# Kernel optimization log

Hardware: AMD Instinct MI355X
Metric: run time of the kernel (lower is better)

The kernel has to match this reference:

```python
import jax, jax.numpy as jnp
import numpy as np

N, E, G, F = 100000, 3200000, 256, 15
NEG_SLOPE = 0.2


def _lin(k, fi, fo):
    s = 1.0 / np.sqrt(fi)
    return jax.random.uniform(k, (fi, fo), jnp.float32, -s, s)


def _vec(k, n, fi):
    s = 1.0 / np.sqrt(fi)
    return jax.random.uniform(k, (n,), jnp.float32, -s, s)


def setup_inputs() -> dict:
    key = jax.random.key(0)
    ks = jax.random.split(key, 40)
    inp = {}
    inp["x"] = jax.random.normal(ks[0], (N, F), jnp.float32)
    inp["edge_index"] = jax.random.randint(ks[1], (2, E), 0, N, dtype=jnp.int32)
    inp["batch"] = jnp.sort(jax.random.randint(ks[2], (N,), 0, G, dtype=jnp.int32))
    inp["xA"] = jax.random.normal(ks[3], (G, 300), jnp.float32)
    i = 4
    for l in (1, 2, 3):
        inp[f"cW{l}"] = _lin(ks[i], F, F); i += 1
        inp[f"cas{l}"] = _vec(ks[i], F, F); i += 1
        inp[f"cad{l}"] = _vec(ks[i], F, F); i += 1
        inp[f"cb{l}"] = jnp.zeros((F,), jnp.float32)
        inp[f"fW{l}"] = _lin(ks[i], F, F); i += 1
        inp[f"fb{l}"] = _vec(ks[i], F, F); i += 1
    inp["m1W"] = _lin(ks[i], 90, 90); i += 1
    inp["m1b"] = _vec(ks[i], 90, 90); i += 1
    inp["aW1"] = _lin(ks[i], 300, 300); i += 1
    inp["ab1"] = _vec(ks[i], 300, 300); i += 1
    inp["aW2"] = _lin(ks[i], 300, 300); i += 1
    inp["ab2"] = _vec(ks[i], 300, 300); i += 1
    inp["aW3"] = _lin(ks[i], 300, 300); i += 1
    inp["ab3"] = _vec(ks[i], 300, 300); i += 1
    inp["aW4"] = _lin(ks[i], 300, 45); i += 1
    inp["ab4"] = _vec(ks[i], 45, 300); i += 1
    inp["m2W"] = _lin(ks[i], 90, 1); i += 1
    inp["m2b"] = _vec(ks[i], 1, 90); i += 1
    return inp


def _gat(x, src, dst, W, a_s, a_d, b):
    """PyG GATConv (heads=1, add_self_loops handled by caller via src/dst)."""
    h = x @ W                                        # [N, F]
    e = jax.nn.leaky_relu((h @ a_s)[src] + (h @ a_d)[dst], NEG_SLOPE)  # [E+N]
    mx = jax.ops.segment_max(e, dst, num_segments=N)
    ex = jnp.exp(e - mx[dst])
    den = jax.ops.segment_sum(ex, dst, num_segments=N)
    alpha = ex / (den[dst] + 1e-16)                   # segment softmax over dst
    out = jax.ops.segment_sum(h[src] * alpha[:, None], dst, num_segments=N)
    return out + b


def reference(x, edge_index, batch, xA,
              cW1, cas1, cad1, cb1, fW1, fb1,
              cW2, cas2, cad2, cb2, fW2, fb2,
              cW3, cas3, cad3, cb3, fW3, fb3,
              m1W, m1b, aW1, ab1, aW2, ab2, aW3, ab3, aW4, ab4,
              m2W, m2b):
    loop = jnp.arange(N, dtype=edge_index.dtype)      # self loops
    src = jnp.concatenate([edge_index[0], loop])
    dst = jnp.concatenate([edge_index[1], loop])

    h = _gat(x, src, dst, cW1, cas1, cad1, cb1)
    h = jax.nn.relu(h @ fW1 + fb1)
    h = _gat(h, src, dst, cW2, cas2, cad2, cb2)
    h = jax.nn.relu(h @ fW2 + fb2)
    h = _gat(h, src, dst, cW3, cas3, cad3, cb3)
    h = h @ fW3 + fb3

    s = jax.ops.segment_sum(h, batch, num_segments=G)
    mx = jax.ops.segment_max(h, batch, num_segments=G)
    cnt = jax.ops.segment_sum(jnp.ones((N, 1), h.dtype), batch, num_segments=G)
    mean = s / jnp.maximum(cnt, 1.0)
    pooled = jnp.concatenate([s, mx, mean], axis=1)   # [G, 45]

    a = jax.nn.relu(xA @ aW1 + ab1)
    a = jax.nn.relu(a @ aW2 + ab2)
    a = jax.nn.sigmoid(a @ aW3 + ab3)
    xann = a @ aW4 + ab4                              # [G, 45]

    z = jnp.concatenate([pooled, xann], axis=1)       # [G, 90]
    z = jax.nn.relu(z @ m1W + m1b)
    z = z @ m2W + m2b
    return jax.nn.sigmoid(z)
```

## Files before the change

kernel.cpp:

```cpp
#include <hip/hip_runtime.h>
#include <hip/hip_bf16.h>
#include <math.h>

#define FDIM 15
#define FPAD 16
#define NEG_SLOPE 0.2f
#define BSH 8
#define BWID 256
#define HB_GRID 256
#define HB_BLK 1024

typedef _Float16 half_t;

__device__ __forceinline__ float leaky(float e) {
  return fmaxf(NEG_SLOPE * e, e);
}

__global__ void k_zero(int* __restrict__ p, int n) {
  int i = blockIdx.x * blockDim.x + threadIdx.x;
  if (i < n) p[i] = 0;
}

__global__ void k_bhist(const int* __restrict__ dstI, int* __restrict__ bcnt,
                        int* __restrict__ bhistG,
                        int n_tot, int n_real, int NB) {
  __shared__ int hist[512];
  int tid = threadIdx.x;
  for (int i = tid; i < NB; i += blockDim.x) hist[i] = 0;
  __syncthreads();
  int stride = gridDim.x * blockDim.x;
  for (int i = blockIdx.x * blockDim.x + tid; i < n_tot; i += stride) {
    int d = (i < n_real) ? dstI[i] : (i - n_real);
    atomicAdd(&hist[d >> BSH], 1);
  }
  __syncthreads();
  for (int i = tid; i < NB; i += blockDim.x) {
    int h = hist[i];
    bhistG[blockIdx.x * 512 + i] = h;
    if (h) atomicAdd(&bcnt[i], h);
  }
}

__global__ void k_bscan(const int* __restrict__ bcnt, int* __restrict__ boff,
                        int* __restrict__ bcur, int* __restrict__ rowptr,
                        int NB, int N, int total) {
  __shared__ int s[512];
  int tid = threadIdx.x;
  int v = (tid < NB) ? bcnt[tid] : 0;
  s[tid] = v;
  __syncthreads();
  for (int off = 1; off < 512; off <<= 1) {
    int add = (tid >= off) ? s[tid - off] : 0;
    __syncthreads();
    s[tid] += add;
    __syncthreads();
  }
  if (tid < NB) { int e = s[tid] - v; boff[tid] = e; bcur[tid] = e; }
  if (tid == NB - 1) boff[NB] = s[tid];
  if (tid == 0) rowptr[N] = total;
}

__global__ void k_bpart(const int* __restrict__ srcI, const int* __restrict__ dstI,
                        int* __restrict__ bcur, int* __restrict__ bbuf,
                        const int* __restrict__ bhistG,
                        int n_tot, int n_real, int NB) {
  __shared__ int hist[512];
  __shared__ int base[512];
  int tid = threadIdx.x;
  for (int i = tid; i < NB; i += blockDim.x) {
    int h = bhistG[blockIdx.x * 512 + i];
    base[i] = h ? atomicAdd(&bcur[i], h) : 0;
    hist[i] = 0;
  }
  __syncthreads();
  int stride = gridDim.x * blockDim.x;
  int g0 = blockIdx.x * blockDim.x + tid;
  for (int i = g0; i < n_tot; i += stride) {
    int s, d;
    if (i < n_real) { s = srcI[i]; d = dstI[i]; }
    else { s = d = i - n_real; }
    int b = d >> BSH;
    int p = base[b] + atomicAdd(&hist[b], 1);
    bbuf[p] = (s << BSH) | (d & (BWID - 1));
  }
}

__global__ void k_bbuild(const int* __restrict__ boff, const int* __restrict__ bbuf,
                         int* __restrict__ rowptr, int* __restrict__ csr, int N) {
  __shared__ int hist[BWID];
  __shared__ int sc[BWID];
  int b = blockIdx.x;
  int tid = threadIdx.x;
  int base_dst = b << BSH;
  int nd = min(BWID, N - base_dst);
  int s0 = boff[b], s1 = boff[b + 1];
  if (tid < BWID) hist[tid] = 0;
  __syncthreads();
  for (int j = s0 + tid; j < s1; j += 512)
    atomicAdd(&hist[bbuf[j] & (BWID - 1)], 1);
  __syncthreads();
  int v = 0;
  if (tid < BWID) { v = hist[tid]; sc[tid] = v; }
  __syncthreads();
  for (int off = 1; off < BWID; off <<= 1) {
    int add = 0;
    if (tid < BWID && tid >= off) add = sc[tid - off];
    __syncthreads();
    if (tid < BWID) sc[tid] += add;
    __syncthreads();
  }
  if (tid < nd) rowptr[base_dst + tid] = s0 + sc[tid] - v;
  __syncthreads();
  if (tid < BWID) hist[tid] = sc[tid] - v;
  __syncthreads();
  for (int j = s0 + tid; j < s1; j += 512) {
    int e = bbuf[j];
    int dl = e & (BWID - 1);
    int p = s0 + atomicAdd(&hist[dl], 1);
    csr[p] = (e >> BSH) << 5;
  }
}

__global__ void k_transform(const float* __restrict__ in, int ld_in,
                            const float* __restrict__ W,
                            const float* __restrict__ a_s,
                            const float* __restrict__ a_d,
                            half_t* __restrict__ hp,
                            float* __restrict__ ad_,
                            int n_nodes) {
  __shared__ float Ws[FDIM * FDIM];
  __shared__ float asv[FDIM], adv[FDIM];
  int tid = threadIdx.x;
  if (tid < FDIM * FDIM) Ws[tid] = W[tid];
  if (tid < FDIM) { asv[tid] = a_s[tid]; adv[tid] = a_d[tid]; }
  __syncthreads();
  int n = blockIdx.x * blockDim.x + tid;
  if (n >= n_nodes) return;
  float xin[FDIM];
#pragma unroll
  for (int j = 0; j < FDIM; ++j) xin[j] = in[n * ld_in + j];
  float sa = 0.f, da = 0.f;
  half_t hrow[FPAD];
#pragma unroll
  for (int o = 0; o < FDIM; ++o) {
    float acc = 0.f;
#pragma unroll
    for (int k = 0; k < FDIM; ++k) acc += xin[k] * Ws[k * FDIM + o];
    hrow[o] = (half_t)acc;
    sa += acc * asv[o];
    da += acc * adv[o];
  }
  hrow[FDIM] = (half_t)sa;
  ad_[n] = da;
  float4 w0, w1;
  __builtin_memcpy(&w0, &hrow[0], 16);
  __builtin_memcpy(&w1, &hrow[8], 16);
  float4* dst = (float4*)(hp + (size_t)n * FPAD);
  dst[0] = w0;
  dst[1] = w1;
}

__device__ __forceinline__ void mlp_rider(int g, int tid, int nthreads,
                                          const float* __restrict__ mIn,
                                          const float* __restrict__ mW,
                                          const float* __restrict__ mB,
                                          float* __restrict__ mOut,
                                          int Nout, int mAct,
                                          float* mins) {
  for (int k = tid; k < 300; k += nthreads) mins[k] = mIn[(size_t)g * 300 + k];
  __syncthreads();
  int j1 = tid;
  int j2 = tid + nthreads;
  bool p1 = (j1 < Nout), p2 = (j2 < Nout);
  if (!p1) return;
  float a0 = 0.f, a1 = 0.f, a2 = 0.f, a3 = 0.f;
  float a4 = 0.f, a5 = 0.f, a6 = 0.f, a7 = 0.f;
  float b0 = 0.f, b1 = 0.f, b2 = 0.f, b3 = 0.f;
  float b4 = 0.f, b5 = 0.f, b6 = 0.f, b7 = 0.f;
  int k = 0;
  for (; k + 7 < 300; k += 8) {
    float i0 = mins[k],     i1 = mins[k + 1], i2 = mins[k + 2], i3 = mins[k + 3];
    float i4 = mins[k + 4], i5 = mins[k + 5], i6 = mins[k + 6], i7 = mins[k + 7];
    float w0 = mW[k * Nout + j1];
    float w1 = mW[(k + 1) * Nout + j1];
    float w2 = mW[(k + 2) * Nout + j1];
    float w3 = mW[(k + 3) * Nout + j1];
    float w4 = mW[(k + 4) * Nout + j1];
    float w5 = mW[(k + 5) * Nout + j1];
    float w6 = mW[(k + 6) * Nout + j1];
    float w7 = mW[(k + 7) * Nout + j1];
    a0 += i0 * w0; a1 += i1 * w1; a2 += i2 * w2; a3 += i3 * w3;
    a4 += i4 * w4; a5 += i5 * w5; a6 += i6 * w6; a7 += i7 * w7;
    if (p2) {
      float v0 = mW[k * Nout + j2];
      float v1 = mW[(k + 1) * Nout + j2];
      float v2 = mW[(k + 2) * Nout + j2];
      float v3 = mW[(k + 3) * Nout + j2];
      float v4 = mW[(k + 4) * Nout + j2];
      float v5 = mW[(k + 5) * Nout + j2];
      float v6 = mW[(k + 6) * Nout + j2];
      float v7 = mW[(k + 7) * Nout + j2];
      b0 += i0 * v0; b1 += i1 * v1; b2 += i2 * v2; b3 += i3 * v3;
      b4 += i4 * v4; b5 += i5 * v5; b6 += i6 * v6; b7 += i7 * v7;
    }
  }
  for (; k < 300; ++k) {
    float ik = mins[k];
    a0 += ik * mW[k * Nout + j1];
    if (p2) b0 += ik * mW[k * Nout + j2];
  }
  float r1 = mB[j1] + ((a0 + a1) + (a2 + a3)) + ((a4 + a5) + (a6 + a7));
  if (mAct == 1) r1 = fmaxf(r1, 0.f);
  else if (mAct == 2) r1 = 1.f / (1.f + expf(-r1));
  mOut[(size_t)g * Nout + j1] = r1;
  if (p2) {
    float r2 = mB[j2] + ((b0 + b1) + (b2 + b3)) + ((b4 + b5) + (b6 + b7));
    if (mAct == 1) r2 = fmaxf(r2, 0.f);
    else if (mAct == 2) r2 = 1.f / (1.f + expf(-r2));
    mOut[(size_t)g * Nout + j2] = r2;
  }
}

__global__ void k_gat(const int* __restrict__ rowptr, const int* __restrict__ csrB,
                      const half_t* __restrict__ hp, const float* __restrict__ ad_,
                      const float* __restrict__ cb, const float* __restrict__ fW,
                      const float* __restrict__ fb,
                      const float* __restrict__ nW, const float* __restrict__ nas,
                      const float* __restrict__ nad,
                      half_t* __restrict__ hp2, float* __restrict__ ad2,
                      float* __restrict__ fout,
                      const float* __restrict__ mIn, const float* __restrict__ mW,
                      const float* __restrict__ mB, float* __restrict__ mOut,
                      int mNout, int mAct, int mlpG,
                      int n_nodes, int do_relu, int fuse) {
  __shared__ float Ws[FDIM * FDIM];
  __shared__ float W2s[FDIM * FDIM];
  __shared__ float cbv[FDIM], fbv[FDIM], as2v[FDIM], ad2v[FDIM];
  __shared__ float cbW[16];
  __shared__ float aggT[16][16];
  __shared__ float outT[16][16];
  __shared__ float mins[304];
  int tid = threadIdx.x;

  if ((int)blockIdx.x < mlpG) {
    mlp_rider(blockIdx.x, tid, blockDim.x, mIn, mW, mB, mOut, mNout, mAct, mins);
    return;
  }

  if (tid < FDIM * FDIM) Ws[tid] = fW[tid];
  if (tid < FDIM) { cbv[tid] = cb[tid]; fbv[tid] = fb[tid]; }
  if (fuse) {
    if (tid < FDIM * FDIM) W2s[tid] = nW[tid];
    if (tid < FDIM) { as2v[tid] = nas[tid]; ad2v[tid] = nad[tid]; }
  }
  __syncthreads();
  if (tid < 16) {
    float s = 0.f;
    if (tid < FDIM) {
#pragma unroll
      for (int k = 0; k < FDIM; ++k) s += cbv[k] * Ws[k * FDIM + tid];
    }
    cbW[tid] = s;
  }
  int dl = tid >> 4;
  int f  = tid & 15;
  int d  = ((int)blockIdx.x - mlpG) * 16 + dl;
  if (d < n_nodes) {
    int rs = rowptr[d], re = rowptr[d + 1];
    int rlast = re - 1;
    float adv = ad_[d];
    const char* hb = (const char*)hp;
    float acc[16];
#pragma unroll
    for (int k = 0; k < 16; ++k) acc[k] = 0.f;

    int i0 = rs + f;
    int oA = csrB[i0 < re ? i0 : rlast];
    uint4 aLo = *(const uint4*)(hb + oA);
    uint4 aHi = *(const uint4*)(hb + oA + 16);
    int i1 = i0 + 16;
    int oB = csrB[i1 < re ? i1 : rlast];

    for (int j = rs; j < re; j += 16) {
      uint4 bLo = *(const uint4*)(hb + oB);
      uint4 bHi = *(const uint4*)(hb + oB + 16);
      int i2 = j + 32 + f;
      int oC = csrB[i2 < re ? i2 : rlast];
      half_t hv[16];
      __builtin_memcpy(hv, &aLo, 16);
      __builtin_memcpy(hv + 8, &aHi, 16);
      float sa = (float)hv[15];
      float w = (j + f < re) ? __expf(leaky(sa + adv)) : 0.f;
#pragma unroll
      for (int k = 0; k < FDIM; ++k) acc[k] += w * (float)hv[k];
      acc[15] += w;
      aLo = bLo; aHi = bHi; oB = oC;
    }

    {
      bool hi = (f & 1);
#pragma unroll
      for (int i = 0; i < 8; ++i) {
        float send = hi ? acc[i] : acc[8 + i];
        float got = __shfl_xor(send, 1, 16);
        acc[i] = (hi ? acc[8 + i] : acc[i]) + got;
      }
      hi = (f & 2);
#pragma unroll
      for (int i = 0; i < 4; ++i) {
        float send = hi ? acc[i] : acc[4 + i];
        float got = __shfl_xor(send, 2, 16);
        acc[i] = (hi ? acc[4 + i] : acc[i]) + got;
      }
      hi = (f & 4);
#pragma unroll
      for (int i = 0; i < 2; ++i) {
        float send = hi ? acc[i] : acc[2 + i];
        float got = __shfl_xor(send, 4, 16);
        acc[i] = (hi ? acc[2 + i] : acc[i]) + got;
      }
      hi = (f & 8);
      {
        float send = hi ? acc[0] : acc[1];
        float got = __shfl_xor(send, 8, 16);
        acc[0] = (hi ? acc[1] : acc[0]) + got;
      }
    }
    int fb = ((f & 1) << 3) | ((f & 2) << 1) | ((f & 4) >> 1) | ((f & 8) >> 3);
    aggT[dl][fb] = acc[0];
  }
  __syncthreads();
  int o = f;
  float ffn = 0.f;
  if (o < FDIM && d < n_nodes) {
    float inv = 1.f / (aggT[dl][15] + 1e-16f);
    float s = 0.f;
#pragma unroll
    for (int k = 0; k < FDIM; ++k) s += aggT[dl][k] * Ws[k * FDIM + o];
    ffn = fbv[o] + cbW[o] + s * inv;
    if (do_relu) ffn = fmaxf(ffn, 0.f);
  }
  if (!fuse) {
    if (d < n_nodes) fout[d * FPAD + o] = (o < FDIM) ? ffn : 0.f;
    return;
  }
  outT[dl][o] = ffn;
  __syncthreads();
  if (d < n_nodes) {
    float h2 = 0.f;
    if (o < FDIM) {
#pragma unroll
      for (int k = 0; k < FDIM; ++k) h2 += outT[dl][k] * W2s[k * FDIM + o];
    }
    float pa = (o < FDIM) ? h2 * as2v[o] : 0.f;
    float pd = (o < FDIM) ? h2 * ad2v[o] : 0.f;
#pragma unroll
    for (int k = 8; k; k >>= 1) {
      pa += __shfl_xor(pa, k, 16);
      pd += __shfl_xor(pd, k, 16);
    }
    hp2[(size_t)d * FPAD + o] = (half_t)((o < FDIM) ? h2 : pa);
    if (o == 0) ad2[d] = pd;
  }
}

__device__ __forceinline__ int lowerb(const int* __restrict__ a, int n, int key) {
  int lo = 0, hi = n;
  while (lo < hi) { int mid = (lo + hi) >> 1; if (a[mid] < key) lo = mid + 1; else hi = mid; }
  return lo;
}

__global__ void k_pool(const float* __restrict__ fout, const int* __restrict__ batch,
                       float* __restrict__ pooled,
                       const float* __restrict__ acts,
                       const float* __restrict__ aW4, const float* __restrict__ ab4,
                       float* __restrict__ xann,
                       int n_nodes, int Gn) {
  __shared__ float ss[256], sm[256];
  __shared__ float mins[304];
  int tid = threadIdx.x;
  if ((int)blockIdx.x < Gn) {
    mlp_rider(blockIdx.x, tid, blockDim.x, acts, aW4, ab4, xann, 45, 0, mins);
    return;
  }
  int g = blockIdx.x - Gn;
  int s = lowerb(batch, n_nodes, g);
  int e = lowerb(batch, n_nodes, g + 1);
  int f = tid & 15;
  float sum = 0.f, mx = -INFINITY;
  for (int n = s + (tid >> 4); n < e; n += 16) {
    float v = fout[n * FPAD + f];
    sum += v;
    mx = fmaxf(mx, v);
  }
  ss[tid] = sum; sm[tid] = mx;
  __syncthreads();
  for (int step = 128; step >= 16; step >>= 1) {
    if (tid < step) { ss[tid] += ss[tid + step]; sm[tid] = fmaxf(sm[tid], sm[tid + step]); }
    __syncthreads();
  }
  if (tid < FDIM) {
    float cnt = (float)(e - s);
    float sv = ss[tid];
    pooled[g * 45 + tid] = sv;
    pooled[g * 45 + 15 + tid] = sm[tid];
    pooled[g * 45 + 30 + tid] = sv / fmaxf(cnt, 1.f);
  }
}

__global__ void k_final(const float* __restrict__ pooled, const float* __restrict__ xann,
                        const float* __restrict__ m1W, const float* __restrict__ m1b,
                        const float* __restrict__ m2W, const float* __restrict__ m2b,
                        float* __restrict__ out) {
  __shared__ float z[90];
  __shared__ float z2[90];
  __shared__ float ps[128];
  int g = blockIdx.x;
  int t = threadIdx.x;
  if (t < 45) z[t] = pooled[g * 45 + t];
  else if (t < 90) z[t] = xann[g * 45 + (t - 45)];
  __syncthreads();
  if (t < 90) {
    float a0 = 0.f, a1 = 0.f;
    for (int k = 0; k < 90; k += 2) {
      float w0 = m1W[k * 90 + t];
      float w1 = m1W[(k + 1) * 90 + t];
      a0 += z[k] * w0; a1 += z[k + 1] * w1;
    }
    z2[t] = fmaxf(m1b[t] + a0 + a1, 0.f);
  }
  __syncthreads();
  if (t < 90) ps[t] = z2[t] * m2W[t];
  else ps[t] = 0.f;
  __syncthreads();
  if (t < 64) {
    float v = ps[t] + ps[t + 64];
#pragma unroll
    for (int k2 = 32; k2; k2 >>= 1) v += __shfl_xor(v, k2, 64);
    if (t == 0) out[g] = 1.f / (1.f + expf(-(v + m2b[0])));
  }
}

extern "C" void kernel_launch(void* const* d_in, const int* in_sizes, int n_in,
                              void* d_out, int out_size, void* d_ws, size_t ws_size,
                              hipStream_t stream) {
  const float* x   = (const float*)d_in[0];
  const int* ei    = (const int*)d_in[1];
  const int* batch = (const int*)d_in[2];
  const float* xA  = (const float*)d_in[3];

  const int N = in_sizes[0] / FDIM;
  const int E = in_sizes[1] / 2;
  const int G = in_sizes[3] / 300;
  const int ET = E + N;
  const int NB = (N + BWID - 1) >> BSH;

  const int* srcI = ei;
  const int* dstI = ei + E;

  float* ws = (float*)d_ws;
  size_t layerW = (size_t)34 * N;
  size_t uSize = layerW > (size_t)ET ? layerW : (size_t)ET;
  size_t off = 0;
  int*    bbuf = (int*)(ws + off);
  half_t* hpA  = (half_t*)(ws + off);
  half_t* hpB  = (half_t*)(ws + off + (size_t)8 * N);
  float*  adA  = ws + off + (size_t)16 * N;
  float*  adB  = ws + off + (size_t)17 * N;
  float*  fout = ws + off + (size_t)18 * N;
  off += uSize;
  int*   rowptr = (int*)(ws + off); off += N + 1;
  int*   csr    = (int*)(ws + off); off += (size_t)ET;
  int*   bcnt   = (int*)(ws + off); off += 516;
  int*   boff   = (int*)(ws + off); off += 516;
  int*   bcur   = (int*)(ws + off); off += 516;
  int*   bhistG = (int*)(ws + off); off += (size_t)512 * HB_GRID;
  float* pooled = ws + off; off += (size_t)G * 45;
  float* a1     = ws + off; off += (size_t)G * 300;
  float* a2     = ws + off; off += (size_t)G * 300;
  float* xann   = ws + off; off += (size_t)G * 45;

  const int B = 256;
  const int gN = (N + B - 1) / B;

  k_zero<<<(NB + B - 1) / B, B, 0, stream>>>(bcnt, NB);
  k_bhist<<<HB_GRID, HB_BLK, 0, stream>>>(dstI, bcnt, bhistG, ET, E, NB);
  k_bscan<<<1, 512, 0, stream>>>(bcnt, boff, bcur, rowptr, NB, N, ET);
  k_bpart<<<HB_GRID, HB_BLK, 0, stream>>>(srcI, dstI, bcur, bbuf, bhistG, ET, E, NB);
  k_bbuild<<<NB, 512, 0, stream>>>(boff, bbuf, rowptr, csr, N);

  const float* cW1  = (const float*)d_in[4];
  const float* cas1 = (const float*)d_in[5];
  const float* cad1 = (const float*)d_in[6];
  const float* cb1  = (const float*)d_in[7];
  const float* fW1  = (const float*)d_in[8];
  const float* fb1  = (const float*)d_in[9];
  const float* cW2  = (const float*)d_in[10];
  const float* cas2 = (const float*)d_in[11];
  const float* cad2 = (const float*)d_in[12];
  const float* cb2  = (const float*)d_in[13];
  const float* fW2  = (const float*)d_in[14];
  const float* fb2  = (const float*)d_in[15];
  const float* cW3  = (const float*)d_in[16];
  const float* cas3 = (const float*)d_in[17];
  const float* cad3 = (const float*)d_in[18];
  const float* cb3  = (const float*)d_in[19];
  const float* fW3  = (const float*)d_in[20];
  const float* fb3  = (const float*)d_in[21];
  const float* m1W  = (const float*)d_in[22];
  const float* m1b  = (const float*)d_in[23];
  const float* aW1  = (const float*)d_in[24];
  const float* ab1  = (const float*)d_in[25];
  const float* aW2  = (const float*)d_in[26];
  const float* ab2  = (const float*)d_in[27];
  const float* aW3  = (const float*)d_in[28];
  const float* ab3  = (const float*)d_in[29];
  const float* aW4  = (const float*)d_in[30];
  const float* ab4  = (const float*)d_in[31];
  const float* m2W  = (const float*)d_in[32];
  const float* m2b  = (const float*)d_in[33];

  const int gGat = (N + 15) / 16;
  k_transform<<<gN, B, 0, stream>>>(x, FDIM, cW1, cas1, cad1, hpA, adA, N);
  k_gat<<<gGat + G, B, 0, stream>>>(rowptr, csr, hpA, adA, cb1, fW1, fb1,
                                    cW2, cas2, cad2, hpB, adB, nullptr,
                                    xA, aW1, ab1, a1, 300, 1, G,
                                    N, 1, 1);
  k_gat<<<gGat + G, B, 0, stream>>>(rowptr, csr, hpB, adB, cb2, fW2, fb2,
                                    cW3, cas3, cad3, hpA, adA, nullptr,
                                    a1, aW2, ab2, a2, 300, 1, G,
                                    N, 1, 1);
  k_gat<<<gGat + G, B, 0, stream>>>(rowptr, csr, hpA, adA, cb3, fW3, fb3,
                                    nullptr, nullptr, nullptr, nullptr, nullptr, fout,
                                    a2, aW3, ab3, a1, 300, 2, G,
                                    N, 0, 0);

  k_pool<<<2 * G, B, 0, stream>>>(fout, batch, pooled, a1, aW4, ab4, xann, N, G);

  k_final<<<G, 128, 0, stream>>>(pooled, xann, m1W, m1b, m2W, m2b, (float*)d_out);
}
```

Baseline: 321.5 us.

## Replace two-level bucketed CSR build with global atomic count, scan, scatter

Drops the bucket-partition CSR construction (per-block bucket histograms, partition into a temporary buffer, per-bucket local sort) and builds the CSR directly. A per-destination global atomic histogram is followed by a three-pass prefix scan, and then an atomic-cursor scatter writes edges straight into the CSR. Self-loops are placed at the end of each row during the scan instead of being pushed through the partition. This removes one full pass over the edges and the intermediate buffer, but adds heavily contended global atomics spread at random over 100K counters. Edge order within each row also becomes nondeterministic, which can change float summation order.

```diff
diff --git a/kernel.cpp b/kernel.cpp
--- a/kernel.cpp
+++ b/kernel.cpp
@@ -5,10 +5,10 @@
 #define FDIM 15
 #define FPAD 16
 #define NEG_SLOPE 0.2f
-#define BSH 8
-#define BWID 256
 #define HB_GRID 256
 #define HB_BLK 1024
+#define SCAN_BLK 1024
+#define SCAN_ELEMS 4096
 
 typedef _Float16 half_t;
 
@@ -21,103 +21,109 @@
   if (i < n) p[i] = 0;
 }
 
-__global__ void k_bhist(const int* __restrict__ dstI, int* __restrict__ bcnt,
-                        int* __restrict__ bhistG,
-                        int n_tot, int n_real, int NB) {
-  __shared__ int hist[512];
-  int tid = threadIdx.x;
-  for (int i = tid; i < NB; i += blockDim.x) hist[i] = 0;
-  __syncthreads();
-  int stride = gridDim.x * blockDim.x;
-  for (int i = blockIdx.x * blockDim.x + tid; i < n_tot; i += stride) {
-    int d = (i < n_real) ? dstI[i] : (i - n_real);
-    atomicAdd(&hist[d >> BSH], 1);
-  }
-  __syncthreads();
-  for (int i = tid; i < NB; i += blockDim.x) {
-    int h = hist[i];
-    bhistG[blockIdx.x * 512 + i] = h;
-    if (h) atomicAdd(&bcnt[i], h);
-  }
-}
-
-__global__ void k_bscan(const int* __restrict__ bcnt, int* __restrict__ boff,
-                        int* __restrict__ bcur, int* __restrict__ rowptr,
-                        int NB, int N, int total) {
-  __shared__ int s[512];
-  int tid = threadIdx.x;
-  int v = (tid < NB) ? bcnt[tid] : 0;
-  s[tid] = v;
-  __syncthreads();
-  for (int off = 1; off < 512; off <<= 1) {
-    int add = (tid >= off) ? s[tid - off] : 0;
+__global__ void k_dhist(const int* __restrict__ dstI, int* __restrict__ rowcnt,
+                        int E, int vec_ok) {
+  int tid = blockIdx.x * blockDim.x + threadIdx.x;
+  int nthr = gridDim.x * blockDim.x;
+  int nv = vec_ok ? (E >> 2) : 0;
+  const int4* d4 = (const int4*)dstI;
+  for (int i = tid; i < nv; i += nthr) {
+    int4 v = d4[i];
+    atomicAdd(&rowcnt[v.x], 1);
+    atomicAdd(&rowcnt[v.y], 1);
+    atomicAdd(&rowcnt[v.z], 1);
+    atomicAdd(&rowcnt[v.w], 1);
+  }
+  for (int i = (nv << 2) + tid; i < E; i += nthr)
+    atomicAdd(&rowcnt[dstI[i]], 1);
+}
+
+__global__ void k_scan1(const int* __restrict__ rowcnt, int* __restrict__ rowptr,
+                        int* __restrict__ blkSum, int N) {
+  __shared__ int ts[SCAN_BLK];
+  int t = threadIdx.x;
+  int base = blockIdx.x * SCAN_ELEMS + t * 4;
+  int v0 = 0, v1 = 0, v2 = 0, v3 = 0;
+  if (base + 3 < N) {
+    int4 c = *(const int4*)(rowcnt + base);
+    v0 = c.x + 1; v1 = c.y + 1; v2 = c.z + 1; v3 = c.w + 1;
+  } else {
+    if (base     < N) v0 = rowcnt[base] + 1;
+    if (base + 1 < N) v1 = rowcnt[base + 1] + 1;
+    if (base + 2 < N) v2 = rowcnt[base + 2] + 1;
+  }
+  int tsum = v0 + v1 + v2 + v3;
+  ts[t] = tsum;
+  __syncthreads();
+  for (int off = 1; off < SCAN_BLK; off <<= 1) {
+    int add = (t >= off) ? ts[t - off] : 0;
     __syncthreads();
-    s[tid] += add;
+    ts[t] += add;
     __syncthreads();
   }
-  if (tid < NB) { int e = s[tid] - v; boff[tid] = e; bcur[tid] = e; }
-  if (tid == NB - 1) boff[NB] = s[tid];
-  if (tid == 0) rowptr[N] = total;
-}
-
-__global__ void k_bpart(const int* __restrict__ srcI, const int* __restrict__ dstI,
-                        int* __restrict__ bcur, int* __restrict__ bbuf,
-                        const int* __restrict__ bhistG,
-                        int n_tot, int n_real, int NB) {
-  __shared__ int hist[512];
-  __shared__ int base[512];
-  int tid = threadIdx.x;
-  for (int i = tid; i < NB; i += blockDim.x) {
-    int h = bhistG[blockIdx.x * 512 + i];
-    base[i] = h ? atomicAdd(&bcur[i], h) : 0;
-    hist[i] = 0;
-  }
-  __syncthreads();
-  int stride = gridDim.x * blockDim.x;
-  int g0 = blockIdx.x * blockDim.x + tid;
-  for (int i = g0; i < n_tot; i += stride) {
-    int s, d;
-    if (i < n_real) { s = srcI[i]; d = dstI[i]; }
-    else { s = d = i - n_real; }
-    int b = d >> BSH;
-    int p = base[b] + atomicAdd(&hist[b], 1);
-    bbuf[p] = (s << BSH) | (d & (BWID - 1));
-  }
-}
-
-__global__ void k_bbuild(const int* __restrict__ boff, const int* __restrict__ bbuf,
-                         int* __restrict__ rowptr, int* __restrict__ csr, int N) {
-  __shared__ int hist[BWID];
-  __shared__ int sc[BWID];
-  int b = blockIdx.x;
-  int tid = threadIdx.x;
-  int base_dst = b << BSH;
-  int nd = min(BWID, N - base_dst);
-  int s0 = boff[b], s1 = boff[b + 1];
-  if (tid < BWID) hist[tid] = 0;
-  __syncthreads();
-  for (int j = s0 + tid; j < s1; j += 512)
-    atomicAdd(&hist[bbuf[j] & (BWID - 1)], 1);
-  __syncthreads();
-  int v = 0;
-  if (tid < BWID) { v = hist[tid]; sc[tid] = v; }
-  __syncthreads();
-  for (int off = 1; off < BWID; off <<= 1) {
-    int add = 0;
-    if (tid < BWID && tid >= off) add = sc[tid - off];
+  int excl = ts[t] - tsum;
+  int p0 = excl, p1 = excl + v0, p2 = p1 + v1, p3 = p2 + v2;
+  if (base + 3 < N) {
+    *(int4*)(rowptr + base) = make_int4(p0, p1, p2, p3);
+  } else {
+    if (base     < N) rowptr[base]     = p0;
+    if (base + 1 < N) rowptr[base + 1] = p1;
+    if (base + 2 < N) rowptr[base + 2] = p2;
+  }
+  if (t == SCAN_BLK - 1) blkSum[blockIdx.x] = ts[t];
+}
+
+__global__ void k_scan2(int* __restrict__ blkSum, int nblk) {
+  __shared__ int s[64];
+  int t = threadIdx.x;
+  int v = (t < nblk) ? blkSum[t] : 0;
+  s[t] = v;
+  __syncthreads();
+  for (int off = 1; off < 64; off <<= 1) {
+    int add = (t >= off) ? s[t - off] : 0;
     __syncthreads();
-    if (tid < BWID) sc[tid] += add;
+    s[t] += add;
     __syncthreads();
   }
-  if (tid < nd) rowptr[base_dst + tid] = s0 + sc[tid] - v;
-  __syncthreads();
-  if (tid < BWID) hist[tid] = sc[tid] - v;
-  __syncthreads();
-  for (int j = s0 + tid; j < s1; j += 512) {
-    int e = bbuf[j];
-    int dl = e & (BWID - 1);
-    int p = s0 + atomicAdd(&hist[dl], 1);
-    csr[p] = (e >> BSH) << 5;
+  if (t < nblk) blkSum[t] = s[t] - v;
+}
+
+__global__ void k_scan3(const int* __restrict__ rowcnt, int* __restrict__ rowptr,
+                        const int* __restrict__ blkSum, int* __restrict__ rcur,
+                        int* __restrict__ csr, int N, int total) {
+  int i = blockIdx.x * blockDim.x + threadIdx.x;
+  if (i >= N) return;
+  int off = blkSum[i / SCAN_ELEMS];
+  int rp = rowptr[i] + off;
+  rowptr[i] = rp;
+  rcur[i] = rp;
+  csr[rp + rowcnt[i]] = i << 5;
+  if (i == N - 1) rowptr[N] = total;
+}
+
+__global__ void k_scatter(const int* __restrict__ srcI, const int* __restrict__ dstI,
+                          int* __restrict__ rcur, int* __restrict__ csr,
+                          int E, int vec_ok) {
+  int tid = blockIdx.x * blockDim.x + threadIdx.x;
+  int nthr = gridDim.x * blockDim.x;
+  int nv = vec_ok ? (E >> 2) : 0;
+  const int4* s4 = (const int4*)srcI;
+  const int4* d4 = (const int4*)dstI;
+  for (int i = tid; i < nv; i += nthr) {
+    int4 s = s4[i];
+    int4 d = d4[i];
+    int p0 = atomicAdd(&rcur[d.x], 1);
+    int p1 = atomicAdd(&rcur[d.y], 1);
+    int p2 = atomicAdd(&rcur[d.z], 1);
+    int p3 = atomicAdd(&rcur[d.w], 1);
+    csr[p0] = s.x << 5;
+    csr[p1] = s.y << 5;
+    csr[p2] = s.z << 5;
+    csr[p3] = s.w << 5;
+  }
+  for (int i = (nv << 2) + tid; i < E; i += nthr) {
+    int p = atomicAdd(&rcur[dstI[i]], 1);
+    csr[p] = srcI[i] << 5;
   }
 }
 
@@ -453,16 +459,17 @@
   const int E = in_sizes[1] / 2;
   const int G = in_sizes[3] / 300;
   const int ET = E + N;
-  const int NB = (N + BWID - 1) >> BSH;
 
   const int* srcI = ei;
   const int* dstI = ei + E;
 
   float* ws = (float*)d_ws;
   size_t layerW = (size_t)34 * N;
-  size_t uSize = layerW > (size_t)ET ? layerW : (size_t)ET;
+  size_t uSize = layerW > (size_t)(2 * N) ? layerW : (size_t)(2 * N);
+  uSize = (uSize + 3) & ~(size_t)3;
   size_t off = 0;
-  int*    bbuf = (int*)(ws + off);
+  int*    rowcnt = (int*)(ws + off);
+  int*    rcur   = (int*)(ws + off) + N;
   half_t* hpA  = (half_t*)(ws + off);
   half_t* hpB  = (half_t*)(ws + off + (size_t)8 * N);
   float*  adA  = ws + off + (size_t)16 * N;
@@ -471,10 +478,7 @@
   off += uSize;
   int*   rowptr = (int*)(ws + off); off += N + 1;
   int*   csr    = (int*)(ws + off); off += (size_t)ET;
-  int*   bcnt   = (int*)(ws + off); off += 516;
-  int*   boff   = (int*)(ws + off); off += 516;
-  int*   bcur   = (int*)(ws + off); off += 516;
-  int*   bhistG = (int*)(ws + off); off += (size_t)512 * HB_GRID;
+  int*   blkSum = (int*)(ws + off); off += 64;
   float* pooled = ws + off; off += (size_t)G * 45;
   float* a1     = ws + off; off += (size_t)G * 300;
   float* a2     = ws + off; off += (size_t)G * 300;
@@ -482,12 +486,15 @@
 
   const int B = 256;
   const int gN = (N + B - 1) / B;
-
-  k_zero<<<(NB + B - 1) / B, B, 0, stream>>>(bcnt, NB);
-  k_bhist<<<HB_GRID, HB_BLK, 0, stream>>>(dstI, bcnt, bhistG, ET, E, NB);
-  k_bscan<<<1, 512, 0, stream>>>(bcnt, boff, bcur, rowptr, NB, N, ET);
-  k_bpart<<<HB_GRID, HB_BLK, 0, stream>>>(srcI, dstI, bcur, bbuf, bhistG, ET, E, NB);
-  k_bbuild<<<NB, 512, 0, stream>>>(boff, bbuf, rowptr, csr, N);
+  const int vec_ok = ((E & 3) == 0) ? 1 : 0;
+  const int nblk = (N + SCAN_ELEMS - 1) / SCAN_ELEMS;
+
+  k_zero<<<(N + B - 1) / B, B, 0, stream>>>(rowcnt, N);
+  k_dhist<<<HB_GRID, HB_BLK, 0, stream>>>(dstI, rowcnt, E, vec_ok);
+  k_scan1<<<nblk, SCAN_BLK, 0, stream>>>(rowcnt, rowptr, blkSum, N);
+  k_scan2<<<1, 64, 0, stream>>>(blkSum, nblk);
+  k_scan3<<<(N + B - 1) / B, B, 0, stream>>>(rowcnt, rowptr, blkSum, rcur, csr, N, ET);
+  k_scatter<<<HB_GRID, HB_BLK, 0, stream>>>(srcI, dstI, rcur, csr, E, vec_ok);
 
   const float* cW1  = (const float*)d_in[4];
   const float* cas1 = (const float*)d_in[5];
```

New measurement: 697.4 us. 2.17x slower.
